# Optimization experiments

Hardware: AMD Instinct MI355X
Metric: run time of the kernel (lower is better)

Reference implementation:

```python
import jax, jax.numpy as jnp
import numpy as np

B, L, D, H = 8, 4096, 512, 512  # batch, seq_len, input channels, hidden_dim
EPS = 1e-5


def setup_inputs() -> dict:
    key = jax.random.key(0)
    ks = jax.random.split(key, 6)
    sD = 1.0 / np.sqrt(D)
    sH = 1.0 / np.sqrt(H)
    return {
        "x": jax.random.normal(ks[0], (B, L, D), jnp.float32),
        "ln_gamma": jnp.ones((D,), jnp.float32),
        "ln_beta": jnp.zeros((D,), jnp.float32),
        "W_B": jax.random.normal(ks[1], (D, H), jnp.float32) * sD,
        "b_B": jnp.zeros((H,), jnp.float32),
        "W_C": jax.random.normal(ks[2], (D, H), jnp.float32) * sD,
        "b_C": jnp.zeros((H,), jnp.float32),
        "W_out": jax.random.normal(ks[3], (H, H), jnp.float32) * sH,
        "b_out": jnp.zeros((H,), jnp.float32),
        # original initializes A to zeros; use decays in (0,1) for a non-trivial scan
        "A": jax.random.uniform(ks[4], (H,), jnp.float32, 0.1, 0.95),
    }


def _scan_op(e1, e2):
    # composition of affine maps h -> a*h + b (elementwise, per channel)
    a1, b1 = e1
    a2, b2 = e2
    return a1 * a2, a2 * b1 + b2


def reference(x, ln_gamma, ln_beta, W_B, b_B, W_C, b_C, W_out, b_out, A):
    # LayerNorm over channels
    mu = jnp.mean(x, axis=-1, keepdims=True)
    var = jnp.var(x, axis=-1, keepdims=True)
    xn = (x - mu) * jax.lax.rsqrt(var + EPS) * ln_gamma + ln_beta  # [B,L,D]

    Bt = jnp.einsum("bld,dh->blh", xn, W_B) + b_B  # [B,L,H]
    Ct = jnp.einsum("bld,dh->blh", xn, W_C) + b_C  # [B,L,H]

    # linear recurrence h_t = A * h_{t-1} + B_t via associative scan over L
    a_full = jnp.broadcast_to(A, Bt.shape)
    _, h = jax.lax.associative_scan(_scan_op, (a_full, Bt), axis=1)  # [B,L,H]

    y = Ct * h  # selective readout
    return jnp.einsum("blh,ho->blo", y, W_out) + b_out  # [B,L,H]
```

## Files before the change

### kernel.cpp

```cpp
#include <hip/hip_runtime.h>
#include <hip/hip_bf16.h>
#include <stdint.h>

typedef __bf16 bf16x8 __attribute__((ext_vector_type(8)));
typedef float f32x4 __attribute__((ext_vector_type(4)));

constexpr int Bn = 8, Ln = 4096, Dn = 512, Hn = 512;
constexpr int Mrows = Bn * Ln;
constexpr int CHUNK = 64, NCHUNK = Ln / CHUNK;

__global__ __launch_bounds__(256) void prep_kernel(
    const float* __restrict__ W_B, const float* __restrict__ W_C,
    const float* __restrict__ W_out, const float* __restrict__ b_B,
    const float* __restrict__ b_C,
    __hip_bfloat16* __restrict__ WbcT, __hip_bfloat16* __restrict__ WoT,
    float* __restrict__ bbc)
{
    int id = blockIdx.x * 256 + threadIdx.x;
    {
        int n = id >> 9, k = id & 511;
        float w = (n < Hn) ? W_B[k * Hn + n] : W_C[k * Hn + (n - Hn)];
        WbcT[id] = __float2bfloat16(w);
    }
    if (id < Hn * Hn) {
        int n = id >> 9, k = id & 511;
        WoT[id] = __float2bfloat16(W_out[k * Hn + n]);
    }
    if (id < 2 * Hn) bbc[id] = (id < Hn) ? b_B[id] : b_C[id - Hn];
}

__global__ __launch_bounds__(256) void ln_kernel(
    const float* __restrict__ x, const float* __restrict__ gamma,
    const float* __restrict__ beta, __hip_bfloat16* __restrict__ xn)
{
    int row = blockIdx.x;
    const float2* xr = reinterpret_cast<const float2*>(x + (size_t)row * Dn);
    int t = threadIdx.x;
    float2 v = xr[t];
    float s = v.x + v.y;
    float s2 = v.x * v.x + v.y * v.y;
    #pragma unroll
    for (int off = 32; off; off >>= 1) {
        s  += __shfl_down(s, off);
        s2 += __shfl_down(s2, off);
    }
    __shared__ float ps[4], ps2[4];
    int wid = t >> 6, lane = t & 63;
    if (lane == 0) { ps[wid] = s; ps2[wid] = s2; }
    __syncthreads();
    float su = ps[0] + ps[1] + ps[2] + ps[3];
    float su2 = ps2[0] + ps2[1] + ps2[2] + ps2[3];
    float mu = su * (1.0f / Dn);
    float var = su2 * (1.0f / Dn) - mu * mu;
    float inv = rsqrtf(var + 1e-5f);
    int c0 = 2 * t;
    float y0 = (v.x - mu) * inv * gamma[c0]     + beta[c0];
    float y1 = (v.y - mu) * inv * gamma[c0 + 1] + beta[c0 + 1];
    __hip_bfloat162 o;
    o.x = __float2bfloat16(y0);
    o.y = __float2bfloat16(y1);
    reinterpret_cast<__hip_bfloat162*>(xn + (size_t)row * Dn)[t] = o;
}

template <int NT, bool OUT_BF16>
__global__ __launch_bounds__(256, 2) void gemm4_kernel(
    const __hip_bfloat16* __restrict__ A,
    const __hip_bfloat16* __restrict__ BT,
    const float* __restrict__ bias,
    void* __restrict__ Cout)
{
    constexpr int K = 512, NIT = 4;
    extern __shared__ unsigned short lds[];

    int nwg = gridDim.x, bid = blockIdx.x;
    int bswz = (bid & 7) * (nwg >> 3) + (bid >> 3);
    constexpr int NBN = NT / 128;
    int bm = bswz / NBN, bnb = bswz % NBN;
    int row0 = bm * 128, col0 = bnb * 128;

    int tid = threadIdx.x;
    int w = tid >> 6, l = tid & 63;
    int rl = l & 15, qg = l >> 4;

    int scol = ((l & 7) ^ (l >> 3)) * 8;
    const __hip_bfloat16* gA = A  + (size_t)(row0 + w * 16 + (l >> 3)) * K + scol;
    const __hip_bfloat16* gB = BT + (size_t)(col0 + w * 16 + (l >> 3)) * K + scol;

#define GLDS(src, dst) __builtin_amdgcn_global_load_lds( \
        (const __attribute__((address_space(1))) void*)(const void*)(src), \
        (__attribute__((address_space(3))) void*)(void*)(dst), 16, 0, 0)
#define STA(b, kt, h, sub) GLDS(gA + (size_t)((h) * 64 + (sub) * 8) * K + (kt) * 64, \
        &lds[(b) * 16384 + (h) * 4096 + w * 1024 + (sub) * 512])
#define STB(b, kt, h, sub) GLDS(gB + (size_t)((h) * 64 + (sub) * 8) * K + (kt) * 64, \
        &lds[(b) * 16384 + 8192 + (h) * 4096 + w * 1024 + (sub) * 512])
#define STAGE_AU(b, kt, h) { STA(b, kt, h, 0); STA(b, kt, h, 1); }
#define STAGE_BU(b, kt, h) { STB(b, kt, h, 0); STB(b, kt, h, 1); }
#define BARRIER { asm volatile("" ::: "memory"); __builtin_amdgcn_s_barrier(); \
                  asm volatile("" ::: "memory"); }
#define VMCNT(n) asm volatile("s_waitcnt vmcnt(" #n ")" ::: "memory")

    int aoff = ((w >> 1) * 64 + rl) * 64;
    int boff = 8192 + ((w & 1) * 64 + rl) * 64;
    int s0k0 = (qg ^ (rl & 7)) * 8;
    int s0k1 = ((4 + qg) ^ (rl & 7)) * 8;

    f32x4 acc[4][4] = {};
    bf16x8 af[2][2], bfr[4][2];

#define RD_A(mq, b) { _Pragma("unroll") for (int i2 = 0; i2 < 2; ++i2) { \
        af[i2][0] = *(const bf16x8*)&lds[(b) * 16384 + aoff + ((mq) * 32 + i2 * 16) * 64 + s0k0]; \
        af[i2][1] = *(const bf16x8*)&lds[(b) * 16384 + aoff + ((mq) * 32 + i2 * 16) * 64 + s0k1]; } }
#define RD_B(nq, b) { _Pragma("unroll") for (int j2 = 0; j2 < 2; ++j2) { \
        bfr[(nq) * 2 + j2][0] = *(const bf16x8*)&lds[(b) * 16384 + boff + ((nq) * 32 + j2 * 16) * 64 + s0k0]; \
        bfr[(nq) * 2 + j2][1] = *(const bf16x8*)&lds[(b) * 16384 + boff + ((nq) * 32 + j2 * 16) * 64 + s0k1]; } }
#define MM(mq, nq) { __builtin_amdgcn_s_setprio(1); \
        _Pragma("unroll") for (int i2 = 0; i2 < 2; ++i2) \
        _Pragma("unroll") for (int j2 = 0; j2 < 2; ++j2) \
        _Pragma("unroll") for (int kk = 0; kk < 2; ++kk) \
            acc[(mq) * 2 + i2][(nq) * 2 + j2] = __builtin_amdgcn_mfma_f32_16x16x32_bf16( \
                af[i2][kk], bfr[(nq) * 2 + j2][kk], acc[(mq) * 2 + i2][(nq) * 2 + j2], 0, 0, 0); \
        __builtin_amdgcn_s_setprio(0); }

    STAGE_BU(0, 0, 0); STAGE_BU(0, 0, 1); STAGE_AU(0, 0, 0); STAGE_AU(0, 0, 1);
    STAGE_BU(1, 1, 0); STAGE_BU(1, 1, 1);
    VMCNT(4);
    BARRIER;

    for (int it = 0; it < NIT; ++it) {
        int e = 2 * it;
        bool more = (it < NIT - 1);
        RD_A(0, 0); RD_B(0, 0);
        STAGE_AU(1, e + 1, 0);
        BARRIER; MM(0, 0); BARRIER;
        RD_B(1, 0);
        STAGE_AU(1, e + 1, 1);
        BARRIER; MM(0, 1); BARRIER;
        RD_A(1, 0);
        if (more) STAGE_BU(0, e + 2, 0);
        BARRIER; MM(1, 1); BARRIER;
        if (more) STAGE_BU(0, e + 2, 1);
        BARRIER; MM(1, 0);
        if (more) { VMCNT(4); } else { VMCNT(0); }
        BARRIER;
        RD_A(0, 1); RD_B(0, 1);
        if (more) STAGE_AU(0, e + 2, 0);
        BARRIER; MM(0, 0); BARRIER;
        RD_B(1, 1);
        if (more) STAGE_AU(0, e + 2, 1);
        BARRIER; MM(0, 1); BARRIER;
        RD_A(1, 1);
        if (more) STAGE_BU(1, e + 3, 0);
        BARRIER; MM(1, 1); BARRIER;
        if (more) {
            STAGE_BU(1, e + 3, 1);
            BARRIER; MM(1, 0); VMCNT(4); BARRIER;
        } else {
            BARRIER; MM(1, 0);
        }
    }

    int crow0 = row0 + (w >> 1) * 64 + qg * 4;
    int ccol0 = col0 + (w & 1) * 64 + rl;
    #pragma unroll
    for (int n = 0; n < 4; ++n) {
        float bv = bias[ccol0 + n * 16];
        #pragma unroll
        for (int i = 0; i < 4; ++i) {
            #pragma unroll
            for (int j = 0; j < 4; ++j) {
                float v = acc[i][n][j] + bv;
                size_t idx = (size_t)(crow0 + i * 16 + j) * NT + (ccol0 + n * 16);
                if (OUT_BF16)
                    ((__hip_bfloat16*)Cout)[idx] = __float2bfloat16(v);
                else
                    ((float*)Cout)[idx] = v;
            }
        }
    }
#undef GLDS
#undef STA
#undef STB
#undef STAGE_AU
#undef STAGE_BU
#undef BARRIER
#undef VMCNT
#undef RD_A
#undef RD_B
#undef MM
}

__global__ __launch_bounds__(256) void scan1_kernel(
    const __hip_bfloat16* __restrict__ BC, const float* __restrict__ Av,
    float* __restrict__ S)
{
    int blk = blockIdx.x;
    int hh = (blk & 1) * 256 + threadIdx.x;
    int c = (blk >> 1) & (NCHUNK - 1);
    int b = blk >> 7;
    float a = Av[hh];
    const __hip_bfloat16* p = BC + ((size_t)(b * Ln + c * CHUNK) * 1024) + hh;
    float s = 0.f;
    #pragma unroll 8
    for (int i = 0; i < CHUNK; ++i) {
        float bv = __bfloat162float(p[(size_t)i * 1024]);
        s = a * s + bv;
    }
    S[((size_t)b * NCHUNK + c) * Hn + hh] = s;
}

__global__ __launch_bounds__(256) void scan2_kernel(
    const float* __restrict__ S, const float* __restrict__ Av,
    float* __restrict__ carry)
{
    int id = blockIdx.x * 256 + threadIdx.x;
    int hh = id & (Hn - 1), b = id >> 9;
    float a = Av[hh];
    float aG = a;
    #pragma unroll
    for (int i = 0; i < 6; ++i) aG *= aG;
    float h = 0.f;
    const float* Sp = S + (size_t)b * NCHUNK * Hn + hh;
    float* cp = carry + (size_t)b * NCHUNK * Hn + hh;
    for (int c = 0; c < NCHUNK; ++c) {
        cp[(size_t)c * Hn] = h;
        h = aG * h + Sp[(size_t)c * Hn];
    }
}

__global__ __launch_bounds__(256) void scan3_kernel(
    const __hip_bfloat16* __restrict__ BC, const float* __restrict__ Av,
    const float* __restrict__ carry, __hip_bfloat16* __restrict__ Y)
{
    int blk = blockIdx.x;
    int hh = (blk & 1) * 256 + threadIdx.x;
    int c = (blk >> 1) & (NCHUNK - 1);
    int b = blk >> 7;
    float a = Av[hh];
    float h = carry[((size_t)b * NCHUNK + c) * Hn + hh];
    const __hip_bfloat16* p = BC + ((size_t)(b * Ln + c * CHUNK) * 1024) + hh;
    __hip_bfloat16* yp = Y + ((size_t)(b * Ln + c * CHUNK) * Hn) + hh;
    #pragma unroll 8
    for (int i = 0; i < CHUNK; ++i) {
        float bv = __bfloat162float(p[(size_t)i * 1024]);
        float cv = __bfloat162float(p[(size_t)i * 1024 + 512]);
        h = a * h + bv;
        yp[(size_t)i * Hn] = __float2bfloat16(cv * h);
    }
}

extern "C" void kernel_launch(void* const* d_in, const int* in_sizes, int n_in,
                              void* d_out, int out_size, void* d_ws, size_t ws_size,
                              hipStream_t stream)
{
    const float* x     = (const float*)d_in[0];
    const float* ln_g  = (const float*)d_in[1];
    const float* ln_b  = (const float*)d_in[2];
    const float* W_B   = (const float*)d_in[3];
    const float* b_B   = (const float*)d_in[4];
    const float* W_C   = (const float*)d_in[5];
    const float* b_C   = (const float*)d_in[6];
    const float* W_out = (const float*)d_in[7];
    const float* b_out = (const float*)d_in[8];
    const float* Avec  = (const float*)d_in[9];

    char* ws = (char*)d_ws;
    __hip_bfloat16* WbcT = (__hip_bfloat16*)(ws);
    __hip_bfloat16* WoT  = (__hip_bfloat16*)(ws + (1u << 20));
    float*          bbc  = (float*)(ws + (1u << 20) + (1u << 19));
    __hip_bfloat16* XN   = (__hip_bfloat16*)(ws + (2u << 20));
    __hip_bfloat16* BC   = (__hip_bfloat16*)(ws + (34u << 20));
    float*          Sbuf = (float*)(ws + (98u << 20));
    float*          Cbuf = (float*)(ws + (99u << 20));
    __hip_bfloat16* Y    = (__hip_bfloat16*)(ws + (100u << 20));

    hipFuncSetAttribute((const void*)gemm4_kernel<1024, true>,
                        hipFuncAttributeMaxDynamicSharedMemorySize, 65536);
    hipFuncSetAttribute((const void*)gemm4_kernel<512, false>,
                        hipFuncAttributeMaxDynamicSharedMemorySize, 65536);

    prep_kernel<<<2048, 256, 0, stream>>>(W_B, W_C, W_out, b_B, b_C, WbcT, WoT, bbc);
    ln_kernel<<<Mrows, 256, 0, stream>>>(x, ln_g, ln_b, XN);
    gemm4_kernel<1024, true><<<(Mrows / 128) * (1024 / 128), 256, 65536, stream>>>(
        XN, WbcT, bbc, BC);
    scan1_kernel<<<Bn * NCHUNK * 2, 256, 0, stream>>>(BC, Avec, Sbuf);
    scan2_kernel<<<(Bn * Hn) / 256, 256, 0, stream>>>(Sbuf, Avec, Cbuf);
    scan3_kernel<<<Bn * NCHUNK * 2, 256, 0, stream>>>(BC, Avec, Cbuf, Y);
    gemm4_kernel<512, false><<<(Mrows / 128) * (512 / 128), 256, 65536, stream>>>(
        Y, WoT, b_out, d_out);
}
```

Before: 136.6 us.

## Fuse chunk-sum scan into GEMM epilogue and merge prep/LN and scan kernels

The first GEMM's epilogue now computes each 64-row chunk's decayed sum of the B projection, using per-lane power weighting and cross-lane shuffles, and writes it straight to the chunk-state buffer. This removes the separate scan1 pass over the BC tensor. The carry-propagation kernel is folded into the final scan kernel, where each block redundantly recomputes its prefix over earlier chunk sums, so the carry buffer and one launch go away. Weight prep and LayerNorm also share one launch. The cost is extra epilogue arithmetic in the GEMM and up to 63 redundant serial iterations per scan block.

New measurement: 137.2 us. Within noise of the previous version (+0.5%).

```diff
diff --git a/kernel.cpp b/kernel.cpp
--- a/kernel.cpp
+++ b/kernel.cpp
@@ -9,33 +9,33 @@
 constexpr int Mrows = Bn * Ln;
 constexpr int CHUNK = 64, NCHUNK = Ln / CHUNK;
 
-__global__ __launch_bounds__(256) void prep_kernel(
+__global__ __launch_bounds__(256) void pre_kernel(
+    const float* __restrict__ x, const float* __restrict__ gamma,
+    const float* __restrict__ beta,
     const float* __restrict__ W_B, const float* __restrict__ W_C,
     const float* __restrict__ W_out, const float* __restrict__ b_B,
     const float* __restrict__ b_C,
+    __hip_bfloat16* __restrict__ xn,
     __hip_bfloat16* __restrict__ WbcT, __hip_bfloat16* __restrict__ WoT,
     float* __restrict__ bbc)
 {
-    int id = blockIdx.x * 256 + threadIdx.x;
-    {
-        int n = id >> 9, k = id & 511;
-        float w = (n < Hn) ? W_B[k * Hn + n] : W_C[k * Hn + (n - Hn)];
-        WbcT[id] = __float2bfloat16(w);
-    }
-    if (id < Hn * Hn) {
-        int n = id >> 9, k = id & 511;
-        WoT[id] = __float2bfloat16(W_out[k * Hn + n]);
-    }
-    if (id < 2 * Hn) bbc[id] = (id < Hn) ? b_B[id] : b_C[id - Hn];
-}
-
-__global__ __launch_bounds__(256) void ln_kernel(
-    const float* __restrict__ x, const float* __restrict__ gamma,
-    const float* __restrict__ beta, __hip_bfloat16* __restrict__ xn)
-{
+    int t = threadIdx.x;
+    if (blockIdx.x >= Mrows) {
+        int id = (blockIdx.x - Mrows) * 256 + t;
+        {
+            int n = id >> 9, k = id & 511;
+            float wv = (n < Hn) ? W_B[k * Hn + n] : W_C[k * Hn + (n - Hn)];
+            WbcT[id] = __float2bfloat16(wv);
+        }
+        if (id < Hn * Hn) {
+            int n = id >> 9, k = id & 511;
+            WoT[id] = __float2bfloat16(W_out[k * Hn + n]);
+        }
+        if (id < 2 * Hn) bbc[id] = (id < Hn) ? b_B[id] : b_C[id - Hn];
+        return;
+    }
     int row = blockIdx.x;
     const float2* xr = reinterpret_cast<const float2*>(x + (size_t)row * Dn);
-    int t = threadIdx.x;
     float2 v = xr[t];
     float s = v.x + v.y;
     float s2 = v.x * v.x + v.y * v.y;
@@ -62,12 +62,13 @@
     reinterpret_cast<__hip_bfloat162*>(xn + (size_t)row * Dn)[t] = o;
 }
 
-template <int NT, bool OUT_BF16>
+template <int NT, bool OUT_BF16, bool WRITE_S>
 __global__ __launch_bounds__(256, 2) void gemm4_kernel(
     const __hip_bfloat16* __restrict__ A,
     const __hip_bfloat16* __restrict__ BT,
     const float* __restrict__ bias,
-    void* __restrict__ Cout)
+    void* __restrict__ Cout,
+    const float* __restrict__ Av, float* __restrict__ Sout)
 {
     constexpr int K = 512, NIT = 4;
     extern __shared__ unsigned short lds[];
@@ -161,20 +162,42 @@
 
     int crow0 = row0 + (w >> 1) * 64 + qg * 4;
     int ccol0 = col0 + (w & 1) * 64 + rl;
+    int cg = (row0 + (w >> 1) * 64) >> 6;
     #pragma unroll
     for (int n = 0; n < 4; ++n) {
-        float bv = bias[ccol0 + n * 16];
+        int col = ccol0 + n * 16;
+        float bv = bias[col];
+        float u[4];
         #pragma unroll
         for (int i = 0; i < 4; ++i) {
+            float uu = 0.f;
             #pragma unroll
             for (int j = 0; j < 4; ++j) {
                 float v = acc[i][n][j] + bv;
-                size_t idx = (size_t)(crow0 + i * 16 + j) * NT + (ccol0 + n * 16);
+                size_t idx = (size_t)(crow0 + i * 16 + j) * NT + col;
                 if (OUT_BF16)
                     ((__hip_bfloat16*)Cout)[idx] = __float2bfloat16(v);
                 else
                     ((float*)Cout)[idx] = v;
+                uu = (j == 0) ? v : (uu * 0.f + v);
             }
+            u[i] = uu;
+        }
+        if (WRITE_S && col0 < 512) {
+            float a = Av[col];
+            float a2 = a * a, a4 = a2 * a2, a8 = a4 * a4, a16 = a8 * a8;
+            #pragma unroll
+            for (int i = 0; i < 4; ++i) {
+                float v0 = acc[i][n][0] + bv, v1 = acc[i][n][1] + bv;
+                float v2 = acc[i][n][2] + bv, v3 = acc[i][n][3] + bv;
+                u[i] = ((v0 * a + v1) * a + v2) * a + v3;
+            }
+            float s = ((u[0] * a16 + u[1]) * a16 + u[2]) * a16 + u[3];
+            float aq = (qg == 0) ? a8 * a4 : (qg == 1) ? a8 : (qg == 2) ? a4 : 1.0f;
+            s *= aq;
+            s += __shfl_xor(s, 16);
+            s += __shfl_xor(s, 32);
+            if (qg == 0) Sout[(size_t)cg * Hn + col] = s;
         }
     }
 #undef GLDS
@@ -189,54 +212,22 @@
 #undef MM
 }
 
-__global__ __launch_bounds__(256) void scan1_kernel(
+__global__ __launch_bounds__(256) void scan_kernel(
     const __hip_bfloat16* __restrict__ BC, const float* __restrict__ Av,
-    float* __restrict__ S)
+    const float* __restrict__ S, __hip_bfloat16* __restrict__ Y)
 {
     int blk = blockIdx.x;
     int hh = (blk & 1) * 256 + threadIdx.x;
     int c = (blk >> 1) & (NCHUNK - 1);
     int b = blk >> 7;
-    float a = Av[hh];
-    const __hip_bfloat16* p = BC + ((size_t)(b * Ln + c * CHUNK) * 1024) + hh;
-    float s = 0.f;
-    #pragma unroll 8
-    for (int i = 0; i < CHUNK; ++i) {
-        float bv = __bfloat162float(p[(size_t)i * 1024]);
-        s = a * s + bv;
-    }
-    S[((size_t)b * NCHUNK + c) * Hn + hh] = s;
-}
-
-__global__ __launch_bounds__(256) void scan2_kernel(
-    const float* __restrict__ S, const float* __restrict__ Av,
-    float* __restrict__ carry)
-{
-    int id = blockIdx.x * 256 + threadIdx.x;
-    int hh = id & (Hn - 1), b = id >> 9;
     float a = Av[hh];
     float aG = a;
     #pragma unroll
     for (int i = 0; i < 6; ++i) aG *= aG;
     float h = 0.f;
     const float* Sp = S + (size_t)b * NCHUNK * Hn + hh;
-    float* cp = carry + (size_t)b * NCHUNK * Hn + hh;
-    for (int c = 0; c < NCHUNK; ++c) {
-        cp[(size_t)c * Hn] = h;
-        h = aG * h + Sp[(size_t)c * Hn];
-    }
-}
-
-__global__ __launch_bounds__(256) void scan3_kernel(
-    const __hip_bfloat16* __restrict__ BC, const float* __restrict__ Av,
-    const float* __restrict__ carry, __hip_bfloat16* __restrict__ Y)
-{
-    int blk = blockIdx.x;
-    int hh = (blk & 1) * 256 + threadIdx.x;
-    int c = (blk >> 1) & (NCHUNK - 1);
-    int b = blk >> 7;
-    float a = Av[hh];
-    float h = carry[((size_t)b * NCHUNK + c) * Hn + hh];
+    for (int cc = 0; cc < c; ++cc)
+        h = aG * h + Sp[(size_t)cc * Hn];
     const __hip_bfloat16* p = BC + ((size_t)(b * Ln + c * CHUNK) * 1024) + hh;
     __hip_bfloat16* yp = Y + ((size_t)(b * Ln + c * CHUNK) * Hn) + hh;
     #pragma unroll 8
@@ -270,21 +261,18 @@
     __hip_bfloat16* XN   = (__hip_bfloat16*)(ws + (2u << 20));
     __hip_bfloat16* BC   = (__hip_bfloat16*)(ws + (34u << 20));
     float*          Sbuf = (float*)(ws + (98u << 20));
-    float*          Cbuf = (float*)(ws + (99u << 20));
     __hip_bfloat16* Y    = (__hip_bfloat16*)(ws + (100u << 20));
 
-    hipFuncSetAttribute((const void*)gemm4_kernel<1024, true>,
+    hipFuncSetAttribute((const void*)gemm4_kernel<1024, true, true>,
                         hipFuncAttributeMaxDynamicSharedMemorySize, 65536);
-    hipFuncSetAttribute((const void*)gemm4_kernel<512, false>,
+    hipFuncSetAttribute((const void*)gemm4_kernel<512, false, false>,
                         hipFuncAttributeMaxDynamicSharedMemorySize, 65536);
 
-    prep_kernel<<<2048, 256, 0, stream>>>(W_B, W_C, W_out, b_B, b_C, WbcT, WoT, bbc);
-    ln_kernel<<<Mrows, 256, 0, stream>>>(x, ln_g, ln_b, XN);
-    gemm4_kernel<1024, true><<<(Mrows / 128) * (1024 / 128), 256, 65536, stream>>>(
-        XN, WbcT, bbc, BC);
-    scan1_kernel<<<Bn * NCHUNK * 2, 256, 0, stream>>>(BC, Avec, Sbuf);
-    scan2_kernel<<<(Bn * Hn) / 256, 256, 0, stream>>>(Sbuf, Avec, Cbuf);
-    scan3_kernel<<<Bn * NCHUNK * 2, 256, 0, stream>>>(BC, Avec, Cbuf, Y);
-    gemm4_kernel<512, false><<<(Mrows / 128) * (512 / 128), 256, 65536, stream>>>(
-        Y, WoT, b_out, d_out);
-}
+    pre_kernel<<<Mrows + 2048, 256, 0, stream>>>(
+        x, ln_g, ln_b, W_B, W_C, W_out, b_B, b_C, XN, WbcT, WoT, bbc);
+    gemm4_kernel<1024, true, true><<<(Mrows / 128) * (1024 / 128), 256, 65536, stream>>>(
+        XN, WbcT, bbc, BC, Avec, Sbuf);
+    scan_kernel<<<Bn * NCHUNK * 2, 256, 0, stream>>>(BC, Avec, Sbuf, Y);
+    gemm4_kernel<512, false, false><<<(Mrows / 128) * (512 / 128), 256, 65536, stream>>>(
+        Y, WoT, b_out, d_out, nullptr, nullptr);
+}
```
